# Kernel tuning notes

Measured on AMD Instinct MI355X. Metric: run time of the kernel, lower is better.

Reference implementation:

```python
import jax, jax.numpy as jnp
import numpy as np

DILATIONS = [[1, 2], [4, 8]]
H = 512      # state_hsize
D_IN = 128   # input_size + exogenous_size
OUT = 48     # output_size
T, B = 256, 128


def _lstm(x, W_ih, W_hh, b_ih, b_hh):
    # x: (T2, B2, D). Standard torch nn.LSTM math, gate order i, f, g, o.
    h0 = jnp.zeros((x.shape[1], W_hh.shape[1]), x.dtype)
    b = b_ih + b_hh

    def step(carry, xt):
        h, c = carry
        g = xt @ W_ih.T + h @ W_hh.T + b
        i, f, gg, o = jnp.split(g, 4, axis=-1)
        c = jax.nn.sigmoid(f) * c + jax.nn.sigmoid(i) * jnp.tanh(gg)
        h = jax.nn.sigmoid(o) * jnp.tanh(c)
        return (h, c), h

    _, ys = jax.lax.scan(step, (h0, h0), x)
    return ys


def _drnn_layer(x, rate, W_ih, W_hh, b_ih, b_hh):
    # Dilated RNN layer: interleave time into the batch dim by `rate`,
    # run a plain LSTM, then de-interleave (zalando DRNN scheme).
    T0, B0, D0 = x.shape
    pad = (-T0) % rate
    if pad:
        x = jnp.concatenate([x, jnp.zeros((pad, B0, D0), x.dtype)], 0)
    Tp = T0 + pad
    dil = x.reshape(Tp // rate, rate * B0, D0)   # dil[t, j*B0+b] = x[t*rate+j, b]
    out = _lstm(dil, W_ih, W_hh, b_ih, b_hh)     # (Tp//rate, rate*B0, H)
    out = out.reshape(Tp // rate, rate, B0, -1).reshape(Tp, B0, -1)
    return out[:T0]


def _forward(input_data, Wih, Whh, bih, bhh, mlp_w, mlp_b, adapter_w, adapter_b):
    x = input_data
    k = 0
    for stack_idx, dils in enumerate(DILATIONS):
        residual = x
        h = x
        for d in dils:
            h = _drnn_layer(h, d, Wih[k], Whh[k], bih[k], bhh[k])
            k += 1
        x = h + residual if stack_idx > 0 else h
    x = jnp.tanh(x @ mlp_w.T + mlp_b)
    return x @ adapter_w.T + adapter_b


def setup_inputs() -> dict:
    key = jax.random.key(0)
    ks = jax.random.split(key, 32)

    def gn(k, shape, s=0.05):
        return (jax.random.normal(k, shape) * s).astype(jnp.float32)

    inp = {"input_data": jax.random.normal(ks[0], (T, B, D_IN), jnp.float32)}
    cell_in = [D_IN, H, H, H]  # input dim of each of the 4 LSTM cells
    for i, d in enumerate(cell_in):
        inp[f"W_ih_{i}"] = gn(ks[1 + 4 * i], (4 * H, d))
        inp[f"W_hh_{i}"] = gn(ks[2 + 4 * i], (4 * H, H))
        inp[f"b_ih_{i}"] = gn(ks[3 + 4 * i], (4 * H,))
        inp[f"b_hh_{i}"] = gn(ks[4 + 4 * i], (4 * H,))
    inp["mlp_w"] = gn(ks[20], (H, H))
    inp["mlp_b"] = gn(ks[21], (H,))
    inp["adapter_w"] = gn(ks[22], (OUT, H))
    inp["adapter_b"] = gn(ks[23], (OUT,))
    return inp


def reference(input_data, W_ih_0, W_hh_0, b_ih_0, b_hh_0,
              W_ih_1, W_hh_1, b_ih_1, b_hh_1,
              W_ih_2, W_hh_2, b_ih_2, b_hh_2,
              W_ih_3, W_hh_3, b_ih_3, b_hh_3,
              mlp_w, mlp_b, adapter_w, adapter_b):
    Wih = [W_ih_0, W_ih_1, W_ih_2, W_ih_3]
    Whh = [W_hh_0, W_hh_1, W_hh_2, W_hh_3]
    bih = [b_ih_0, b_ih_1, b_ih_2, b_ih_3]
    bhh = [b_hh_0, b_hh_1, b_hh_2, b_hh_3]
    return _forward(input_data, Wih, Whh, bih, bhh, mlp_w, mlp_b, adapter_w, adapter_b)
```

## Files before the change

kernel.cpp:

```cpp
#include <hip/hip_runtime.h>

#define TPB 512
#define SPIN_BOUND (1u << 20)

typedef _Float16 h8 __attribute__((ext_vector_type(8)));
typedef float f4 __attribute__((ext_vector_type(4)));
typedef unsigned long long u64;

__device__ __forceinline__ float sigf(float x) { return 1.f / (1.f + __expf(-x)); }
__device__ __forceinline__ float tanhfast(float x) { return 2.f / (1.f + __expf(-2.f * x)) - 1.f; }

#define MF(acc, a, b) acc = __builtin_amdgcn_mfma_f32_16x16x32_f16(a, b, acc, 0, 0, 0)

__device__ __forceinline__ void vm0() { asm volatile("s_waitcnt vmcnt(0)" ::: "memory"); }
__device__ __forceinline__ void l1inv() { asm volatile("buffer_inv sc0" ::: "memory"); }
__device__ __forceinline__ void lgkm0() { asm volatile("s_waitcnt lgkmcnt(0)" ::: "memory"); }



__global__ void prep_conv(const float* __restrict__ in, const float* __restrict__ mlpw,
                          const float* __restrict__ adpw,
                          _Float16* __restrict__ seqX, _Float16* __restrict__ mlpW16,
                          _Float16* __restrict__ adpW16)
{
    const int NIN = 256 * 128 * 128;
    const int NM = 512 * 512;
    const int NA = 48 * 512;
    int i = blockIdx.x * blockDim.x + threadIdx.x;
    const int stride = gridDim.x * blockDim.x;
    for (; i < NIN + NM + NA; i += stride) {
        if (i < NIN) seqX[i] = (_Float16)in[i];
        else if (i < NIN + NM) mlpW16[i - NIN] = (_Float16)mlpw[i - NIN];
        else adpW16[i - NIN - NM] = (_Float16)adpw[i - NIN - NM];
    }
}

__global__ void prep_bias(const float* __restrict__ a0, const float* __restrict__ b0,
                          const float* __restrict__ a1, const float* __restrict__ b1,
                          const float* __restrict__ a2, const float* __restrict__ b2,
                          const float* __restrict__ a3, const float* __restrict__ b3,
                          float* __restrict__ biasSum)
{
    int i = blockIdx.x * blockDim.x + threadIdx.x;
    if (i >= 8192) return;
    const int c = i >> 11, j = i & 2047;
    const float* A = (c == 0) ? a0 : (c == 1) ? a1 : (c == 2) ? a2 : a3;
    const float* B = (c == 0) ? b0 : (c == 1) ? b1 : (c == 2) ? b2 : b3;
    biasSum[i] = A[j] + B[j];
}

__global__ void prep_w(const float* __restrict__ wih0, const float* __restrict__ whh0,
                       const float* __restrict__ wih1, const float* __restrict__ whh1,
                       const float* __restrict__ wih2, const float* __restrict__ whh2,
                       const float* __restrict__ wih3, const float* __restrict__ whh3,
                       _Float16* __restrict__ Wprep)
{
    const size_t N0 = (size_t)2048 * 640;
    const size_t N1 = (size_t)2048 * 1024;
    const size_t total = N0 + 3 * N1;
    size_t i = (size_t)blockIdx.x * blockDim.x + threadIdx.x;
    const size_t stride = (size_t)gridDim.x * blockDim.x;
    for (; i < total; i += stride) {
        int cell; size_t off;
        if (i < N0) { cell = 0; off = i; }
        else { cell = 1 + (int)((i - N0) / N1); off = (i - N0) % N1; }
        const int K = cell ? 1024 : 640;
        const int Din = cell ? 512 : 128;
        const int k = (int)(off % K);
        const int rowIdx = (int)(off / K);
        const int p = rowIdx >> 6;
        const int row64 = rowIdx & 63;
        const int q = row64 >> 4;
        const int gRow = q * 512 + p * 16 + (row64 & 15);
        const float* wih = (cell == 0) ? wih0 : (cell == 1) ? wih1 : (cell == 2) ? wih2 : wih3;
        const float* whh = (cell == 0) ? whh0 : (cell == 1) ? whh1 : (cell == 2) ? whh2 : whh3;
        const float v = (k < Din) ? wih[(size_t)gRow * Din + k]
                                  : whh[(size_t)gRow * 512 + (k - Din)];
        Wprep[i] = (_Float16)v;
    }
}


#define SCR_OFF   131072
#define SCRT_OFF  147456
#define MISC_OFF  151552

template<int CELL, int KH, bool FLAT>
__device__ __forceinline__ void run_cell(
    const _Float16* __restrict__ src, _Float16* __restrict__ dstF,
    _Float16* __restrict__ dstX,
    const _Float16* __restrict__ wbase, const float* __restrict__ biasSum,
    unsigned* __restrict__ cellFlags, char* smem,
    const int rg, const int p, const int tid, const int lane, const int wave)
{
    constexpr int Din = (CELL == 0) ? 128 : 512;
    constexpr int K = Din + 512;
    constexpr int Bd = 128 << CELL;
    constexpr int Td = 256 >> CELL;
    constexpr int r = Bd >> 3;
    constexpr int nMt = r >> 4;
    constexpr int ldsRow = K * 2;
    constexpr int NKX = Din >> 5;
    constexpr int NXW = NKX / KH;
    constexpr int NHW = 16 / KH;
    constexpr int B1 = (NHW > 8) ? 8 : NHW;
    constexpr int B2 = NHW - B1;
    constexpr int NCOMP = nMt * KH;

    const int colsel = lane & 15;
    const int kq = lane >> 4;
    const int rowBase = rg * r;

    {
        const _Float16* wsl = wbase + (size_t)p * 64 * K;
        constexpr int kcN = K >> 3;
        for (int i = tid; i < 64 * kcN; i += TPB) {
            const int row = i / kcN;
            const int kc = i - row * kcN;
            h8 v = *(const h8*)(wsl + (size_t)row * K + (kc << 3));
            *(h8*)(smem + row * ldsRow + ((kc << 4) ^ ((row & 7) << 4))) = v;
        }
    }
    __syncthreads();

    const int mt = wave / KH;
    const int kh = wave % KH;
    const bool busy = (wave < NCOMP);

    const int xlo = kh * NXW;
    const int hlo = kh * NHW;

    const float bq0 = biasSum[CELL * 2048 + 0 * 512 + p * 16 + colsel];
    const float bq1 = biasSum[CELL * 2048 + 1 * 512 + p * 16 + colsel];
    const float bq2 = biasSum[CELL * 2048 + 2 * 512 + p * 16 + colsel];
    const float bq3 = biasSum[CELL * 2048 + 3 * 512 + p * 16 + colsel];

    const int arow = rowBase + mt * 16 + colsel;
    const int hcol = p * 16 + colsel;

    unsigned* line = cellFlags + (rg * 8 + mt) * 256;
    unsigned* myFlag = line + p * 8;
    float* scr = (float*)(smem + SCR_OFF);
    char* scrT = smem + SCRT_OFF + mt * 512;

    float cr[4] = {0.f, 0.f, 0.f, 0.f};
    bool dead = false;
    h8 xr[(NXW > 0) ? NXW : 1];

    const size_t hOff = (size_t)arow * 16 + (size_t)(kq & 1) * 8 + (size_t)(kq >> 1) * Bd * 16;

    auto ldB = [&](int kbyte, int rrow) -> h8 {
        return *(const h8*)(smem + rrow * ldsRow + (kbyte ^ ((rrow & 7) << 4)));
    };

    auto wait_line = [&](unsigned tgt) {
        if (dead) return;
        const volatile unsigned* fp = (const volatile unsigned*)(line + (lane & 31) * 8);
        unsigned n = 0;
        for (;;) {
            if (__all((int)(*fp >= tgt))) return;
            l1inv();
            __builtin_amdgcn_s_sleep(1);
            if (++n > SPIN_BOUND) { dead = true; return; }
        }
    };
    auto wait_own = [&](unsigned tgt) {
        if (dead) return;
        const volatile unsigned* f0 = (const volatile unsigned*)myFlag;
        if (*f0 >= tgt) return;
        unsigned n = 0;
        for (;;) {
            l1inv();
            if (*f0 >= tgt) return;
            __builtin_amdgcn_s_sleep(1);
            if (++n > SPIN_BOUND) { dead = true; return; }
        }
    };

    auto x_issue = [&](int t) {
        const _Float16* ap = src + (size_t)t * Bd * Din + (size_t)arow * Din + (kq << 3);
        #pragma unroll
        for (int i = 0; i < NXW; ++i)
            xr[i] = *(const h8*)(ap + ((xlo + i) << 5));
    };
    auto x_compute = [&](f4 (&C)[4]) {
        #pragma unroll
        for (int g = 0; g < 4; ++g) C[g] = (f4){0.f, 0.f, 0.f, 0.f};
        #pragma unroll
        for (int i = 0; i < NXW; ++i) {
            const int kbyte = (((xlo + i) << 5) + (kq << 3)) << 1;
            h8 bf0 = ldB(kbyte, colsel);
            h8 bf1 = ldB(kbyte, 16 + colsel);
            h8 bf2 = ldB(kbyte, 32 + colsel);
            h8 bf3 = ldB(kbyte, 48 + colsel);
            MF(C[0], xr[i], bf0); MF(C[1], xr[i], bf1);
            MF(C[2], xr[i], bf2); MF(C[3], xr[i], bf3);
        }
    };
    auto h_mfma = [&](h8 a, int ks, f4 (&C)[4]) {
        const int kbyte = (Din + (ks << 5) + (kq << 3)) << 1;
        h8 bf0 = ldB(kbyte, colsel);
        h8 bf1 = ldB(kbyte, 16 + colsel);
        h8 bf2 = ldB(kbyte, 32 + colsel);
        h8 bf3 = ldB(kbyte, 48 + colsel);
        MF(C[0], a, bf0); MF(C[1], a, bf1); MF(C[2], a, bf2); MF(C[3], a, bf3);
    };
    auto writeScr = [&](f4 (&C)[4]) {
        const int slot = (mt * (KH - 1) + (kh - 1)) * 4;
        #pragma unroll
        for (int g = 0; g < 4; ++g)
            *(f4*)(scr + (size_t)((slot + g) * 64 + lane) * 4) = C[g];
    };
    auto finish = [&](int t, f4 (&C)[4]) {
        if constexpr (KH > 1) {
            #pragma unroll
            for (int s = 0; s < KH - 1; ++s)
                #pragma unroll
                for (int g = 0; g < 4; ++g)
                    C[g] += *(const f4*)(scr + (size_t)(((mt * (KH - 1) + s) * 4 + g) * 64 + lane) * 4);
        }
        _Float16 hf[4];
        #pragma unroll
        for (int j = 0; j < 4; ++j) {
            const float gi = C[0][j] + bq0;
            const float gf = C[1][j] + bq1;
            const float gg = C[2][j] + bq2;
            const float go = C[3][j] + bq3;
            const float cc = sigf(gf) * cr[j] + sigf(gi) * tanhfast(gg);
            cr[j] = cc;
            hf[j] = (_Float16)(sigf(go) * tanhfast(cc));
        }
        #pragma unroll
        for (int j = 0; j < 4; ++j)
            *(_Float16*)(scrT + (kq * 4 + j) * 32 + colsel * 2) = hf[j];
        lgkm0();
        const u64 v = *(const u64*)(scrT + (lane >> 2) * 32 + (lane & 3) * 8);
        const size_t Ebase = ((size_t)t * 32 + p) * (size_t)(Bd * 16)
                           + (size_t)(rowBase + mt * 16) * 16;
        *(u64*)((char*)dstX + Ebase * 2 + (size_t)lane * 8) = v;
        vm0();
        if (lane == 0) *(volatile unsigned*)myFlag = (unsigned)(t + 1);
        if constexpr (FLAT) {
            const size_t rb = (size_t)t * Bd + rowBase + mt * 16 + kq * 4;
            #pragma unroll
            for (int j = 0; j < 4; ++j)
                dstF[(rb + j) * 512 + hcol] = hf[j];
        }
    };

    f4 acc[4];
    h8 hrA[B1];
    h8 hrB[(B2 > 0) ? B2 : 1];
    if (busy) x_issue(0);

    for (int t = 0; t < Td; ++t) {
        const char* hXp = (const char*)dstX + ((size_t)(t - 1) * 32 * Bd * 16 + hOff) * 2;
        if (busy && t > 0) {
            if constexpr (KH > 1) { if (kh != 0) wait_own((unsigned)t); }
            wait_line((unsigned)t);
            #pragma unroll
            for (int i = 0; i < B1; ++i)
                hrA[i] = *(const h8*)(hXp + (size_t)(hlo + i) * (Bd * 64));
        }
        if (busy) {
            x_compute(acc);
            if (t > 0) {
                if constexpr (B2 > 0) {
                    #pragma unroll
                    for (int i = 0; i < B2; ++i)
                        hrB[i] = *(const h8*)(hXp + (size_t)(hlo + B1 + i) * (Bd * 64));
                }
                #pragma unroll
                for (int i = 0; i < B1; ++i) h_mfma(hrA[i], hlo + i, acc);
                if constexpr (B2 > 0) {
                    #pragma unroll
                    for (int i = 0; i < B2; ++i) h_mfma(hrB[i], hlo + B1 + i, acc);
                }
            }
        }
        if constexpr (KH > 1) {
            if (busy && kh != 0) writeScr(acc);
            __syncthreads();
        }
        if (busy && kh == 0) finish(t, acc);
        if (busy && t + 1 < Td) x_issue(t + 1);
    }
    vm0();
}


__global__ __launch_bounds__(TPB) void drnn_persist(
    const _Float16* __restrict__ seqX,
    _Float16* __restrict__ seq0F, _Float16* __restrict__ seq0X,
    _Float16* __restrict__ seq1F, _Float16* __restrict__ seq1X,
    _Float16* __restrict__ seq2F, _Float16* __restrict__ seq2X,
    _Float16* __restrict__ seq3X,
    const _Float16* __restrict__ Wprep,
    const float* __restrict__ biasSum,
    unsigned* __restrict__ syncc)
{
    extern __shared__ char smem[];
    const int tid = threadIdx.x;
    const int lane = tid & 63;
    const int wave = tid >> 6;

    unsigned* s_misc = (unsigned*)(smem + MISC_OFF);

    if (tid == 0) {
        unsigned xcc;
        asm volatile("s_getreg_b32 %0, hwreg(HW_REG_XCC_ID)" : "=s"(xcc));
        xcc &= 7u;
        unsigned slot = __hip_atomic_fetch_add(syncc + 512u + 64u * xcc, 1u,
                                               __ATOMIC_RELAXED, __HIP_MEMORY_SCOPE_AGENT);
        s_misc[0] = (xcc << 5) | (slot & 31u);
    }
    __syncthreads();
    const unsigned rgp = s_misc[0];
    __syncthreads();
    const int rg = rgp >> 5;
    const int p = rgp & 31;

    unsigned* cellCnt = syncc;
    unsigned* flags = syncc + 4096;

    auto cell_barrier = [&](int cellIdx, unsigned TdPrev, int nMtPrev, unsigned* flagsPrev) {
        __syncthreads();
        if (p == 0 && tid < 32 * nMtPrev) {
            const volatile unsigned* fp =
                (const volatile unsigned*)(flagsPrev + (rg * 8 + (tid >> 5)) * 256 + (tid & 31) * 8);
            unsigned n = 0;
            for (;;) {
                l1inv();
                if (*fp >= TdPrev) break;
                __builtin_amdgcn_s_sleep(1);
                if (++n > SPIN_BOUND) break;
            }
        }
        __syncthreads();
        if (tid == 0) {
            if (p == 0)
                __hip_atomic_fetch_add(cellCnt, 1u, __ATOMIC_RELEASE, __HIP_MEMORY_SCOPE_AGENT);
            unsigned n = 0;
            while (__hip_atomic_load(cellCnt, __ATOMIC_RELAXED, __HIP_MEMORY_SCOPE_AGENT)
                   < (unsigned)(8 * cellIdx)) {
                __builtin_amdgcn_s_sleep(1);
                if (++n > SPIN_BOUND) break;
            }
            (void)__hip_atomic_load(cellCnt, __ATOMIC_ACQUIRE, __HIP_MEMORY_SCOPE_AGENT);
        }
        __syncthreads();
        l1inv();
    };

    run_cell<0, 2, true >(seqX,  seq0F, seq0X, Wprep,                        biasSum, flags + 0 * 16384, smem, rg, p, tid, lane, wave);
    cell_barrier(1, 256u, 1, flags + 0 * 16384);
    run_cell<1, 2, true >(seq0F, seq1F, seq1X, Wprep + (size_t)2048 * 640,   biasSum, flags + 1 * 16384, smem, rg, p, tid, lane, wave);
    cell_barrier(2, 128u, 2, flags + 1 * 16384);
    run_cell<2, 2, true >(seq1F, seq2F, seq2X, Wprep + (size_t)2048 * 1664,  biasSum, flags + 2 * 16384, smem, rg, p, tid, lane, wave);
    cell_barrier(3, 64u, 4, flags + 2 * 16384);
    run_cell<3, 1, false>(seq2F, nullptr, seq3X, Wprep + (size_t)2048 * 2688, biasSum, flags + 3 * 16384, smem, rg, p, tid, lane, wave);
}


__global__ __launch_bounds__(256) void head_kernel(
    const _Float16* __restrict__ seq1,
    const _Float16* __restrict__ seq3X,
    const _Float16* __restrict__ mlpW16,
    const float* __restrict__ mlp_b,
    const _Float16* __restrict__ adpW16,
    const float* __restrict__ adp_b,
    float* __restrict__ out)
{
    extern __shared__ char smem[];
    const int tid = threadIdx.x;
    const int lane = tid & 63, wave = tid >> 6;
    const int colsel = lane & 15, kq = lane >> 4;
    const size_t row0 = (size_t)blockIdx.x * 64 + wave * 16;

    h8 aR[16];
    {
        const size_t R = row0 + colsel;
        const size_t ar = R * 512;
        const size_t off3 = ((R >> 10) * 32 + (size_t)(kq >> 1)) * 16384
                          + (R & 1023) * 16 + (size_t)(kq & 1) * 8;
        #pragma unroll
        for (int ks = 0; ks < 16; ++ks) {
            const int kb = ks * 32 + kq * 8;
            h8 a1 = *(const h8*)(seq1 + ar + kb);
            h8 a3 = *(const h8*)(seq3X + off3 + (size_t)ks * 32768);
            aR[ks] = a1 + a3;
        }
    }
    for (int nt = 0; nt < 32; ++nt) {
        f4 acc = {0.f, 0.f, 0.f, 0.f};
        const int brow = nt * 16 + colsel;
        #pragma unroll
        for (int ks = 0; ks < 16; ++ks) {
            const int kb = ks * 32 + kq * 8;
            h8 b = *(const h8*)(mlpW16 + (size_t)brow * 512 + kb);
            acc = __builtin_amdgcn_mfma_f32_16x16x32_f16(aR[ks], b, acc, 0, 0, 0);
        }
        const int n = nt * 16 + colsel;
        const float bn = mlp_b[n];
        const int lrow0 = wave * 16 + kq * 4;
        #pragma unroll
        for (int j = 0; j < 4; ++j) {
            const float y = tanhfast(acc[j] + bn);
            const int row = lrow0 + j;
            *(_Float16*)(smem + row * 1024 + ((n * 2) ^ ((row & 7) << 4))) = (_Float16)y;
        }
    }
    __syncthreads();
    f4 acc0 = {0.f,0.f,0.f,0.f}, acc1 = {0.f,0.f,0.f,0.f}, acc2 = {0.f,0.f,0.f,0.f};
    const int arow = wave * 16 + colsel;
    #pragma unroll
    for (int ks = 0; ks < 16; ++ks) {
        const int kb = ks * 32 + kq * 8;
        h8 a = *(const h8*)(smem + arow * 1024 + ((kb * 2) ^ ((arow & 7) << 4)));
        h8 b0 = *(const h8*)(adpW16 + (size_t)(colsel) * 512 + kb);
        h8 b1 = *(const h8*)(adpW16 + (size_t)(16 + colsel) * 512 + kb);
        h8 b2 = *(const h8*)(adpW16 + (size_t)(32 + colsel) * 512 + kb);
        acc0 = __builtin_amdgcn_mfma_f32_16x16x32_f16(a, b0, acc0, 0, 0, 0);
        acc1 = __builtin_amdgcn_mfma_f32_16x16x32_f16(a, b1, acc1, 0, 0, 0);
        acc2 = __builtin_amdgcn_mfma_f32_16x16x32_f16(a, b2, acc2, 0, 0, 0);
    }
    const size_t orow0 = row0 + kq * 4;
    #pragma unroll
    for (int j = 0; j < 4; ++j) {
        out[(orow0 + j) * 48 + colsel]      = acc0[j] + adp_b[colsel];
        out[(orow0 + j) * 48 + 16 + colsel] = acc1[j] + adp_b[16 + colsel];
        out[(orow0 + j) * 48 + 32 + colsel] = acc2[j] + adp_b[32 + colsel];
    }
}


extern "C" void kernel_launch(void* const* d_in, const int* in_sizes, int n_in,
                              void* d_out, int out_size, void* d_ws, size_t ws_size,
                              hipStream_t stream)
{
    (void)in_sizes; (void)n_in; (void)out_size; (void)ws_size;
    const float* input = (const float*)d_in[0];
    const float* Wih[4]; const float* Whh[4]; const float* Bih[4]; const float* Bhh[4];
    for (int i = 0; i < 4; ++i) {
        Wih[i] = (const float*)d_in[1 + 4 * i];
        Whh[i] = (const float*)d_in[2 + 4 * i];
        Bih[i] = (const float*)d_in[3 + 4 * i];
        Bhh[i] = (const float*)d_in[4 + 4 * i];
    }
    const float* mlpw = (const float*)d_in[17];
    const float* mlpb = (const float*)d_in[18];
    const float* adpw = (const float*)d_in[19];
    const float* adpb = (const float*)d_in[20];
    float* out = (float*)d_out;

    char* ws = (char*)d_ws;
    size_t off = 0;
    auto alloc = [&](size_t bytes) -> char* {
        char* ptr = ws + off;
        off += (bytes + 255) & ~(size_t)255;
        return ptr;
    };
    const size_t SEQB = (size_t)32768 * 512 * 2;
    const size_t SYNC_BYTES = (size_t)(4096 + 4 * 16384) * 4;
    unsigned* syncc   = (unsigned*)alloc(SYNC_BYTES);
    _Float16* seqX    = (_Float16*)alloc((size_t)32768 * 128 * 2);
    _Float16* seq0F   = (_Float16*)alloc(SEQB);
    _Float16* seq0X   = (_Float16*)alloc(SEQB);
    _Float16* seq1F   = (_Float16*)alloc(SEQB);
    _Float16* seq1X   = (_Float16*)alloc(SEQB);
    _Float16* seq2F   = (_Float16*)alloc(SEQB);
    _Float16* seq2X   = (_Float16*)alloc(SEQB);
    _Float16* seq3X   = (_Float16*)alloc(SEQB);
    _Float16* Wprep   = (_Float16*)alloc((size_t)2048 * 3712 * 2);
    float*    biasSum = (float*)alloc(8192 * 4);
    _Float16* mlpW16  = (_Float16*)alloc((size_t)262144 * 2);
    _Float16* adpW16  = (_Float16*)alloc((size_t)24576 * 2);

    hipMemsetAsync(syncc, 0, SYNC_BYTES, stream);
    prep_conv<<<2048, 256, 0, stream>>>(input, mlpw, adpw, seqX, mlpW16, adpW16);
    prep_bias<<<32, 256, 0, stream>>>(Bih[0], Bhh[0], Bih[1], Bhh[1],
                                      Bih[2], Bhh[2], Bih[3], Bhh[3], biasSum);
    prep_w<<<4096, 256, 0, stream>>>(Wih[0], Whh[0], Wih[1], Whh[1],
                                     Wih[2], Whh[2], Wih[3], Whh[3], Wprep);

    const int ldsBytes = MISC_OFF + 128;
    hipFuncSetAttribute((const void*)drnn_persist,
                        hipFuncAttributeMaxDynamicSharedMemorySize, ldsBytes);
    hipFuncSetAttribute((const void*)head_kernel,
                        hipFuncAttributeMaxDynamicSharedMemorySize, 65536);

    drnn_persist<<<256, TPB, ldsBytes, stream>>>(seqX, seq0F, seq0X, seq1F, seq1X,
                                                 seq2F, seq2X, seq3X,
                                                 Wprep, biasSum, syncc);
    head_kernel<<<512, 256, 65536, stream>>>(seq1F, seq3X, mlpW16, mlpb, adpW16, adpb, out);
}
```

Measured before the change: 2.170 ms.

## Drop flat sequence copies; read next cell inputs from exchange-layout buffers

Removes the extra row-major (flat) fp16 output write in each LSTM cell. The following cell and the head kernel now read their inputs directly from the tiled exchange buffer already used for the hidden-state handoff, with index math that maps the dilation interleave onto that layout. This cuts global store traffic and workspace on the recurrent critical path. In exchange the input loads become strided across tiles, which may coalesce less well.

```diff
diff --git a/kernel.cpp b/kernel.cpp
--- a/kernel.cpp
+++ b/kernel.cpp
@@ -85,10 +85,9 @@
 #define SCRT_OFF  147456
 #define MISC_OFF  151552
 
-template<int CELL, int KH, bool FLAT>
+template<int CELL, int KH, bool XH>
 __device__ __forceinline__ void run_cell(
-    const _Float16* __restrict__ src, _Float16* __restrict__ dstF,
-    _Float16* __restrict__ dstX,
+    const _Float16* __restrict__ src, _Float16* __restrict__ dstX,
     const _Float16* __restrict__ wbase, const float* __restrict__ biasSum,
     unsigned* __restrict__ cellFlags, char* smem,
     const int rg, const int p, const int tid, const int lane, const int wave)
@@ -96,6 +95,7 @@
     constexpr int Din = (CELL == 0) ? 128 : 512;
     constexpr int K = Din + 512;
     constexpr int Bd = 128 << CELL;
+    constexpr int PBd = Bd / 2;
     constexpr int Td = 256 >> CELL;
     constexpr int r = Bd >> 3;
     constexpr int nMt = r >> 4;
@@ -136,7 +136,6 @@
     const float bq3 = biasSum[CELL * 2048 + 3 * 512 + p * 16 + colsel];
 
     const int arow = rowBase + mt * 16 + colsel;
-    const int hcol = p * 16 + colsel;
 
     unsigned* line = cellFlags + (rg * 8 + mt) * 256;
     unsigned* myFlag = line + p * 8;
@@ -147,7 +146,10 @@
     bool dead = false;
     h8 xr[(NXW > 0) ? NXW : 1];
 
-    const size_t hOff = (size_t)arow * 16 + (size_t)(kq & 1) * 8 + (size_t)(kq >> 1) * Bd * 16;
+    const size_t hOff = (size_t)arow * 16 + (size_t)(kq & 1) * 8 + (size_t)(kq >> 1) * (Bd * 16);
+    const int tOff = (arow >= PBd) ? 1 : 0;
+    const size_t xBase = (size_t)(arow - tOff * PBd) * 16
+                       + (size_t)(kq & 1) * 8 + (size_t)(kq >> 1) * (PBd * 16);
 
     auto ldB = [&](int kbyte, int rrow) -> h8 {
         return *(const h8*)(smem + rrow * ldsRow + (kbyte ^ ((rrow & 7) << 4)));
@@ -178,10 +180,18 @@
     };
 
     auto x_issue = [&](int t) {
-        const _Float16* ap = src + (size_t)t * Bd * Din + (size_t)arow * Din + (kq << 3);
-        #pragma unroll
-        for (int i = 0; i < NXW; ++i)
-            xr[i] = *(const h8*)(ap + ((xlo + i) << 5));
+        if constexpr (XH) {
+            const char* xp = (const char*)src
+                + ((size_t)(2 * t + tOff) * (32 * PBd * 16) + xBase) * 2;
+            #pragma unroll
+            for (int i = 0; i < NXW; ++i)
+                xr[i] = *(const h8*)(xp + (size_t)(xlo + i) * (PBd * 64));
+        } else {
+            const _Float16* ap = src + (size_t)t * Bd * Din + (size_t)arow * Din + (kq << 3);
+            #pragma unroll
+            for (int i = 0; i < NXW; ++i)
+                xr[i] = *(const h8*)(ap + ((xlo + i) << 5));
+        }
     };
     auto x_compute = [&](f4 (&C)[4]) {
         #pragma unroll
@@ -240,12 +250,6 @@
         *(u64*)((char*)dstX + Ebase * 2 + (size_t)lane * 8) = v;
         vm0();
         if (lane == 0) *(volatile unsigned*)myFlag = (unsigned)(t + 1);
-        if constexpr (FLAT) {
-            const size_t rb = (size_t)t * Bd + rowBase + mt * 16 + kq * 4;
-            #pragma unroll
-            for (int j = 0; j < 4; ++j)
-                dstF[(rb + j) * 512 + hcol] = hf[j];
-        }
     };
 
     f4 acc[4];
@@ -254,7 +258,7 @@
     if (busy) x_issue(0);
 
     for (int t = 0; t < Td; ++t) {
-        const char* hXp = (const char*)dstX + ((size_t)(t - 1) * 32 * Bd * 16 + hOff) * 2;
+        const char* hXp = (const char*)dstX + ((size_t)(t - 1) * (32 * Bd * 16) + hOff) * 2;
         if (busy && t > 0) {
             if constexpr (KH > 1) { if (kh != 0) wait_own((unsigned)t); }
             wait_line((unsigned)t);
@@ -291,9 +295,9 @@
 
 __global__ __launch_bounds__(TPB) void drnn_persist(
     const _Float16* __restrict__ seqX,
-    _Float16* __restrict__ seq0F, _Float16* __restrict__ seq0X,
-    _Float16* __restrict__ seq1F, _Float16* __restrict__ seq1X,
-    _Float16* __restrict__ seq2F, _Float16* __restrict__ seq2X,
+    _Float16* __restrict__ seq0X,
+    _Float16* __restrict__ seq1X,
+    _Float16* __restrict__ seq2X,
     _Float16* __restrict__ seq3X,
     const _Float16* __restrict__ Wprep,
     const float* __restrict__ biasSum,
@@ -352,18 +356,18 @@
         l1inv();
     };
 
-    run_cell<0, 2, true >(seqX,  seq0F, seq0X, Wprep,                        biasSum, flags + 0 * 16384, smem, rg, p, tid, lane, wave);
+    run_cell<0, 2, false>(seqX,  seq0X, Wprep,                        biasSum, flags + 0 * 16384, smem, rg, p, tid, lane, wave);
     cell_barrier(1, 256u, 1, flags + 0 * 16384);
-    run_cell<1, 2, true >(seq0F, seq1F, seq1X, Wprep + (size_t)2048 * 640,   biasSum, flags + 1 * 16384, smem, rg, p, tid, lane, wave);
+    run_cell<1, 2, true >(seq0X, seq1X, Wprep + (size_t)2048 * 640,   biasSum, flags + 1 * 16384, smem, rg, p, tid, lane, wave);
     cell_barrier(2, 128u, 2, flags + 1 * 16384);
-    run_cell<2, 2, true >(seq1F, seq2F, seq2X, Wprep + (size_t)2048 * 1664,  biasSum, flags + 2 * 16384, smem, rg, p, tid, lane, wave);
+    run_cell<2, 2, true >(seq1X, seq2X, Wprep + (size_t)2048 * 1664,  biasSum, flags + 2 * 16384, smem, rg, p, tid, lane, wave);
     cell_barrier(3, 64u, 4, flags + 2 * 16384);
-    run_cell<3, 1, false>(seq2F, nullptr, seq3X, Wprep + (size_t)2048 * 2688, biasSum, flags + 3 * 16384, smem, rg, p, tid, lane, wave);
+    run_cell<3, 1, true >(seq2X, seq3X, Wprep + (size_t)2048 * 2688,  biasSum, flags + 3 * 16384, smem, rg, p, tid, lane, wave);
 }
 
 
 __global__ __launch_bounds__(256) void head_kernel(
-    const _Float16* __restrict__ seq1,
+    const _Float16* __restrict__ seq1X,
     const _Float16* __restrict__ seq3X,
     const _Float16* __restrict__ mlpW16,
     const float* __restrict__ mlp_b,
@@ -380,13 +384,13 @@
     h8 aR[16];
     {
         const size_t R = row0 + colsel;
-        const size_t ar = R * 512;
+        const size_t off1 = ((R >> 8) * 32 + (size_t)(kq >> 1)) * 4096
+                          + (R & 255) * 16 + (size_t)(kq & 1) * 8;
         const size_t off3 = ((R >> 10) * 32 + (size_t)(kq >> 1)) * 16384
                           + (R & 1023) * 16 + (size_t)(kq & 1) * 8;
         #pragma unroll
         for (int ks = 0; ks < 16; ++ks) {
-            const int kb = ks * 32 + kq * 8;
-            h8 a1 = *(const h8*)(seq1 + ar + kb);
+            h8 a1 = *(const h8*)(seq1X + off1 + (size_t)ks * 8192);
             h8 a3 = *(const h8*)(seq3X + off3 + (size_t)ks * 32768);
             aR[ks] = a1 + a3;
         }
@@ -464,11 +468,8 @@
     const size_t SYNC_BYTES = (size_t)(4096 + 4 * 16384) * 4;
     unsigned* syncc   = (unsigned*)alloc(SYNC_BYTES);
     _Float16* seqX    = (_Float16*)alloc((size_t)32768 * 128 * 2);
-    _Float16* seq0F   = (_Float16*)alloc(SEQB);
     _Float16* seq0X   = (_Float16*)alloc(SEQB);
-    _Float16* seq1F   = (_Float16*)alloc(SEQB);
     _Float16* seq1X   = (_Float16*)alloc(SEQB);
-    _Float16* seq2F   = (_Float16*)alloc(SEQB);
     _Float16* seq2X   = (_Float16*)alloc(SEQB);
     _Float16* seq3X   = (_Float16*)alloc(SEQB);
     _Float16* Wprep   = (_Float16*)alloc((size_t)2048 * 3712 * 2);
@@ -489,8 +490,7 @@
     hipFuncSetAttribute((const void*)head_kernel,
                         hipFuncAttributeMaxDynamicSharedMemorySize, 65536);
 
-    drnn_persist<<<256, TPB, ldsBytes, stream>>>(seqX, seq0F, seq0X, seq1F, seq1X,
-                                                 seq2F, seq2X, seq3X,
+    drnn_persist<<<256, TPB, ldsBytes, stream>>>(seqX, seq0X, seq1X, seq2X, seq3X,
                                                  Wprep, biasSum, syncc);
-    head_kernel<<<512, 256, 65536, stream>>>(seq1F, seq3X, mlpW16, mlpb, adpW16, adpb, out);
-}
+    head_kernel<<<512, 256, 65536, stream>>>(seq1X, seq3X, mlpW16, mlpb, adpW16, adpb, out);
+}
```

Measured after the change: 2.002 ms (median of 2 runs). -7.7%, faster.
